# Kernel tuning notes

Hardware: AMD Instinct MI355X
Metric: run time of the kernel (lower is better)

Reference implementation:

```python
import jax, jax.numpy as jnp
import numpy as np

GROUP_SIZE = 64
M, K, N, RANK = 4096, 4096, 4096, 32


def setup_inputs() -> dict:
    key = jax.random.key(0)
    ks = jax.random.split(key, 7)
    x = jax.random.normal(ks[0], (M, K), dtype=jnp.float32)
    # int4 weight residual in [-8, 7]
    q_w = jax.random.randint(ks[1], (K, N), -8, 8, dtype=jnp.int32)
    # positive per-group weight scales, shape (K // group_size, N)
    wscales = jax.random.uniform(ks[2], (K // GROUP_SIZE, N), dtype=jnp.float32) * 0.01 + 1e-4
    lora_down = jax.random.normal(ks[3], (K, RANK), dtype=jnp.float32) * 0.02
    lora_up = jax.random.normal(ks[4], (RANK, N), dtype=jnp.float32) * 0.02
    # smoothing factors, strictly positive
    smooth = jax.random.uniform(ks[5], (K,), dtype=jnp.float32) + 0.5
    bias = jax.random.normal(ks[6], (N,), dtype=jnp.float32)
    return {"x": x, "q_w": q_w, "wscales": wscales, "lora_down": lora_down,
            "lora_up": lora_up, "smooth": smooth, "bias": bias}


def reference(x, q_w, wscales, lora_down, lora_up, smooth, bias):
    G = GROUP_SIZE
    m, k = x.shape
    n = q_w.shape[1]
    ng = k // G  # groups along K

    # smooth activation: move outliers into weights
    x_smooth = x / smooth[None, :]

    # per-group symmetric int4 quantize + dequantize of activations
    xg = x_smooth.reshape(m, ng, G)
    ascales = jnp.maximum(jnp.max(jnp.abs(xg), axis=-1) / 7.0, 1e-8)  # (m, ng)
    qx = jnp.clip(jnp.round(xg / ascales[..., None]), -8.0, 7.0)
    x_dq = (qx * ascales[..., None]).reshape(m, k)

    # dequantize int4 weight residual: grouped along K
    W_dq = (q_w.astype(jnp.float32).reshape(ng, G, n) * wscales[:, None, :]).reshape(k, n)

    # simulated int4 GEMM + fp LoRA residual + bias
    y_main = x_dq @ W_dq
    y_lora = (x @ lora_down) @ lora_up
    return y_main + y_lora + bias[None, :]
```

## Files before the change

### kernel.cpp

```cpp
#include <hip/hip_runtime.h>
#include <hip/hip_bf16.h>
#include <stdint.h>

#define GSIZE 64
#define MDIM 4096
#define KDIM 4096
#define NDIM 4096
#define RANK 32
#define KE   4160
#define NG   64
#define NSPLIT 8

#define N_LORAT (32 * NSPLIT)
#define B_WPREP0 N_LORAT
#define N_WPREP (65 * 64)
#define B_QUANT0 (B_WPREP0 + N_WPREP)
#define NBLOCKS  (B_QUANT0 + MDIM)

typedef __bf16 bf16x4 __attribute__((ext_vector_type(4)));
typedef __bf16 bf16x8 __attribute__((ext_vector_type(8)));
typedef float  f32x4  __attribute__((ext_vector_type(4)));

#define GPTR(p) ((__attribute__((address_space(1))) void*)(uintptr_t)(p))
#define LPTR(p) ((__attribute__((address_space(3))) void*)(p))

__global__ __launch_bounds__(256) void k_prep(const float* __restrict__ x,
                                              const int*   __restrict__ qw,
                                              const float* __restrict__ wsc,
                                              const float* __restrict__ ld,
                                              const float* __restrict__ lu,
                                              const float* __restrict__ smooth,
                                              __bf16* __restrict__ A,
                                              __bf16* __restrict__ Wt,
                                              float* __restrict__ tws) {
    __shared__ __attribute__((aligned(16))) char smem[10240];
    int b   = blockIdx.x;
    int tid = threadIdx.x;

    if (b < N_LORAT) {
        __bf16* AsL = (__bf16*)smem;
        __bf16* BsL = (__bf16*)(smem + 8192);
        int m0    = (b & 31) * 128;
        int sp    = b >> 5;
        int kbase = sp * 512;
        int lane = tid & 63;
        int wave = tid >> 6;
        int quad = lane >> 4;
        int mrow = lane & 15;

        f32x4 z = {0.f, 0.f, 0.f, 0.f};
        f32x4 acc[2][2];
        acc[0][0] = z; acc[0][1] = z; acc[1][0] = z; acc[1][1] = z;

        for (int step = 0; step < 16; ++step) {
            int kk = kbase + step * 32;
            #pragma unroll
            for (int it = 0; it < 2; ++it) {
                int slot = it * 256 + tid;
                int r = slot >> 2;
                int g = (slot & 3) ^ (r & 3);
                const float* src = x + (size_t)(m0 + r) * KDIM + kk + g * 8;
                float4 a0 = *(const float4*)src;
                float4 a1 = *(const float4*)(src + 4);
                bf16x8 v = {(__bf16)a0.x, (__bf16)a0.y, (__bf16)a0.z, (__bf16)a0.w,
                            (__bf16)a1.x, (__bf16)a1.y, (__bf16)a1.z, (__bf16)a1.w};
                *(bf16x8*)(AsL + slot * 8) = v;
            }
            #pragma unroll
            for (int i2 = 0; i2 < 4; ++i2) {
                int j = i2 * 256 + tid;
                int r = j >> 5, n = j & 31;
                BsL[n * 32 + r] = (__bf16)ld[(size_t)(kk + r) * RANK + n];
            }
            __syncthreads();
            bf16x8 av[2], bv[2];
            #pragma unroll
            for (int i = 0; i < 2; ++i) {
                int row  = wave * 32 + i * 16 + mrow;
                int slot = row * 4 + (quad ^ (row & 3));
                av[i] = *(const bf16x8*)(AsL + slot * 8);
            }
            #pragma unroll
            for (int j = 0; j < 2; ++j)
                bv[j] = *(const bf16x8*)(BsL + (j * 16 + mrow) * 32 + quad * 8);
            #pragma unroll
            for (int i = 0; i < 2; ++i)
                #pragma unroll
                for (int j = 0; j < 2; ++j)
                    acc[i][j] = __builtin_amdgcn_mfma_f32_16x16x32_bf16(av[i], bv[j], acc[i][j], 0, 0, 0);
            __syncthreads();
        }
        float* tout = tws + (size_t)sp * MDIM * RANK;
        #pragma unroll
        for (int i = 0; i < 2; ++i)
            #pragma unroll
            for (int j = 0; j < 2; ++j)
                #pragma unroll
                for (int r = 0; r < 4; ++r) {
                    int rowg = m0 + wave * 32 + i * 16 + quad * 4 + r;
                    int col  = j * 16 + mrow;
                    tout[(size_t)rowg * RANK + col] = acc[i][j][r];
                }
        return;
    }

    if (b < B_QUANT0) {
        __bf16 (*tile)[68] = (__bf16(*)[68])smem;
        int idx = b - B_WPREP0;
        int n0 = (idx & 63) * 64;
        int kt = idx >> 6;
        int k0 = kt * 64;
        int tr = tid >> 4;
        int tc = (tid & 15) * 4;
        if (kt < NG) {
            float4 ws = *(const float4*)(wsc + (size_t)kt * NDIM + n0 + tc);
            #pragma unroll
            for (int r = tr; r < 64; r += 16) {
                int4 q = *(const int4*)(qw + (size_t)(k0 + r) * NDIM + n0 + tc);
                tile[r][tc + 0] = (__bf16)((float)q.x * ws.x);
                tile[r][tc + 1] = (__bf16)((float)q.y * ws.y);
                tile[r][tc + 2] = (__bf16)((float)q.z * ws.z);
                tile[r][tc + 3] = (__bf16)((float)q.w * ws.w);
            }
        } else {
            #pragma unroll
            for (int r = tr; r < 64; r += 16) {
                if (r < RANK) {
                    float4 lv = *(const float4*)(lu + (size_t)r * NDIM + n0 + tc);
                    tile[r][tc + 0] = (__bf16)lv.x;
                    tile[r][tc + 1] = (__bf16)lv.y;
                    tile[r][tc + 2] = (__bf16)lv.z;
                    tile[r][tc + 3] = (__bf16)lv.w;
                } else {
                    tile[r][tc + 0] = (__bf16)0.f;
                    tile[r][tc + 1] = (__bf16)0.f;
                    tile[r][tc + 2] = (__bf16)0.f;
                    tile[r][tc + 3] = (__bf16)0.f;
                }
            }
        }
        __syncthreads();
        int nn = tid >> 3;
        int ks = (tid & 7) * 8;
        #pragma unroll
        for (int p = 0; p < 2; ++p) {
            int n = nn + p * 32;
            bf16x8 v;
            #pragma unroll
            for (int e = 0; e < 8; ++e) v[e] = tile[ks + e][n];
            *(bf16x8*)(Wt + (size_t)(n0 + n) * KE + k0 + ks) = v;
        }
        return;
    }

    {
        int row = b - B_QUANT0;
        const float4* xr4 = (const float4*)(x + (size_t)row * KDIM);
        const float4* sm4 = (const float4*)smooth;
        __bf16* ar = A + (size_t)row * KE;
        #pragma unroll
        for (int p = 0; p < 4; ++p) {
            int i4 = p * 256 + tid;
            float4 xv = xr4[i4];
            float4 sv = sm4[i4];
            float4 xs = {xv.x * __builtin_amdgcn_rcpf(sv.x),
                         xv.y * __builtin_amdgcn_rcpf(sv.y),
                         xv.z * __builtin_amdgcn_rcpf(sv.z),
                         xv.w * __builtin_amdgcn_rcpf(sv.w)};
            float a = fmaxf(fmaxf(fabsf(xs.x), fabsf(xs.y)),
                            fmaxf(fabsf(xs.z), fabsf(xs.w)));
            #pragma unroll
            for (int off = 1; off < 16; off <<= 1)
                a = fmaxf(a, __shfl_xor(a, off, 64));
            float ascale = fmaxf(a * (1.0f / 7.0f), 1e-8f);
            float rin = __builtin_amdgcn_rcpf(ascale);
            float q0 = fminf(fmaxf(rintf(xs.x * rin), -8.f), 7.f);
            float q1 = fminf(fmaxf(rintf(xs.y * rin), -8.f), 7.f);
            float q2 = fminf(fmaxf(rintf(xs.z * rin), -8.f), 7.f);
            float q3 = fminf(fmaxf(rintf(xs.w * rin), -8.f), 7.f);
            bf16x4 av = {(__bf16)(q0 * ascale), (__bf16)(q1 * ascale),
                         (__bf16)(q2 * ascale), (__bf16)(q3 * ascale)};
            *(bf16x4*)(ar + i4 * 4) = av;
        }
    }
}

__global__ __launch_bounds__(256) void k_fin(const float* __restrict__ tws,
                                             __bf16* __restrict__ A) {
    int idx = blockIdx.x * 256 + threadIdx.x;
    int m = idx >> 4, cq = idx & 15;
    int c = cq * 4;
    bf16x4 v = {(__bf16)0.f, (__bf16)0.f, (__bf16)0.f, (__bf16)0.f};
    if (c < RANK) {
        f32x4 s = {0.f, 0.f, 0.f, 0.f};
        #pragma unroll
        for (int sp = 0; sp < NSPLIT; ++sp) {
            f32x4 p = *(const f32x4*)(tws + ((size_t)sp * MDIM + m) * RANK + c);
            s.x += p.x; s.y += p.y; s.z += p.z; s.w += p.w;
        }
        v[0] = (__bf16)s.x; v[1] = (__bf16)s.y; v[2] = (__bf16)s.z; v[3] = (__bf16)s.w;
    }
    *(bf16x4*)(A + (size_t)m * KE + KDIM + c) = v;
}

__global__ __launch_bounds__(256) void k_gemm(const __bf16* __restrict__ A,
                                              const __bf16* __restrict__ Wt,
                                              const float*  __restrict__ bias,
                                              float* __restrict__ out) {
    __shared__ __attribute__((aligned(16))) __bf16 As[128 * 64];
    __shared__ __attribute__((aligned(16))) __bf16 Bs[128 * 64];
    int tid  = threadIdx.x;
    int lane = tid & 63;
    int wave = tid >> 6;
    int quad = lane >> 4;
    int mrow = lane & 15;
    int wm = wave >> 1, wn = wave & 1;
    int m0 = blockIdx.y * 128, n0 = blockIdx.x * 128;

    f32x4 z = {0.f, 0.f, 0.f, 0.f};
    f32x4 acc[4][4];
    #pragma unroll
    for (int i = 0; i < 4; ++i)
        #pragma unroll
        for (int j = 0; j < 4; ++j) acc[i][j] = z;

    const __bf16* Ab = A  + (size_t)m0 * KE;
    const __bf16* Bb = Wt + (size_t)n0 * KE;

    for (int kt = 0; kt < KE / 64; ++kt) {
        int k0 = kt * 64;
        #pragma unroll
        for (int it = 0; it < 4; ++it) {
            int c = it * 256 + tid;
            int r = c >> 3;
            int g = (c & 7) ^ (r & 7);
            int ldsoff = (it * 256 + wave * 64) * 16;
            __builtin_amdgcn_global_load_lds(GPTR(Ab + (size_t)r * KE + k0 + g * 8),
                                             LPTR((char*)As + ldsoff), 16, 0, 0);
            __builtin_amdgcn_global_load_lds(GPTR(Bb + (size_t)r * KE + k0 + g * 8),
                                             LPTR((char*)Bs + ldsoff), 16, 0, 0);
        }
        __syncthreads();
        #pragma unroll
        for (int s = 0; s < 2; ++s) {
            bf16x8 av[4], bv[4];
            #pragma unroll
            for (int i = 0; i < 4; ++i) {
                int row  = wm * 64 + i * 16 + mrow;
                int slot = row * 8 + ((s * 4 + quad) ^ (row & 7));
                av[i] = *(const bf16x8*)(As + slot * 8);
            }
            #pragma unroll
            for (int j = 0; j < 4; ++j) {
                int row  = wn * 64 + j * 16 + mrow;
                int slot = row * 8 + ((s * 4 + quad) ^ (row & 7));
                bv[j] = *(const bf16x8*)(Bs + slot * 8);
            }
            #pragma unroll
            for (int i = 0; i < 4; ++i)
                #pragma unroll
                for (int j = 0; j < 4; ++j)
                    acc[i][j] = __builtin_amdgcn_mfma_f32_16x16x32_bf16(av[i], bv[j], acc[i][j], 0, 0, 0);
        }
        __syncthreads();
    }

    #pragma unroll
    for (int j = 0; j < 4; ++j) {
        int col = n0 + wn * 64 + j * 16 + mrow;
        float bvs = bias[col];
        #pragma unroll
        for (int i = 0; i < 4; ++i) {
            int rbase = m0 + wm * 64 + i * 16 + quad * 4;
            #pragma unroll
            for (int r = 0; r < 4; ++r)
                __builtin_nontemporal_store(acc[i][j][r] + bvs,
                                            &out[(size_t)(rbase + r) * NDIM + col]);
        }
    }
}

extern "C" void kernel_launch(void* const* d_in, const int* in_sizes, int n_in,
                              void* d_out, int out_size, void* d_ws, size_t ws_size,
                              hipStream_t stream) {
    const float* x    = (const float*)d_in[0];
    const int*   qw   = (const int*)  d_in[1];
    const float* wsc  = (const float*)d_in[2];
    const float* ld   = (const float*)d_in[3];
    const float* lu   = (const float*)d_in[4];
    const float* sm   = (const float*)d_in[5];
    const float* bias = (const float*)d_in[6];
    float* out = (float*)d_out;

    char* ws = (char*)d_ws;
    __bf16* A   = (__bf16*)ws;
    __bf16* Wt  = (__bf16*)(ws + (size_t)MDIM * KE * 2);
    float*  tws = (float*) (ws + (size_t)MDIM * KE * 4);

    k_prep<<<NBLOCKS, 256, 0, stream>>>(x, qw, wsc, ld, lu, sm, A, Wt, tws);
    k_fin<<<(MDIM * 16) / 256, 256, 0, stream>>>(tws, A);
    k_gemm<<<dim3(NDIM / 128, MDIM / 128), 256, 0, stream>>>(A, Wt, bias, out);
}
```

Before: 342.0 us.

## Restructure GEMM into 256x256 tiles with double-buffered, phase-interleaved LDS prefetch

The bf16 GEMM moves from 128x128 tiles with 4 waves and a load-sync-compute loop to 256x256 tiles with 8 waves. Each k-step is split into four quadrant phases, and the global-to-LDS loads for the next two k-steps are issued between phases. This double-buffers LDS and overlaps memory with MFMA work using explicit vmcnt waits, barriers and setprio. It cuts global traffic per FLOP, at the cost of 128KB of LDS, heavier register use and fragile hand-tuned synchronisation.

```diff
diff --git a/kernel.cpp b/kernel.cpp
--- a/kernel.cpp
+++ b/kernel.cpp
@@ -203,81 +203,131 @@
     *(bf16x4*)(A + (size_t)m * KE + KDIM + c) = v;
 }
 
-__global__ __launch_bounds__(256) void k_gemm(const __bf16* __restrict__ A,
-                                              const __bf16* __restrict__ Wt,
-                                              const float*  __restrict__ bias,
-                                              float* __restrict__ out) {
-    __shared__ __attribute__((aligned(16))) __bf16 As[128 * 64];
-    __shared__ __attribute__((aligned(16))) __bf16 Bs[128 * 64];
+#define NT (KE / 64)
+#define HS 8192
+#define BS 16384
+
+#define STAGE(ldsbase, gb, kt, half) do {                                     \
+    int _k0 = (kt) * 64;                                                      \
+    _Pragma("unroll")                                                         \
+    for (int _it = 0; _it < 2; ++_it) {                                       \
+        int _c = _it * 512 + tid;                                             \
+        int _r = _c >> 3;                                                     \
+        int _g = (_c & 7) ^ (_r & 7);                                         \
+        __builtin_amdgcn_global_load_lds(                                     \
+            GPTR((gb) + (size_t)((half) * 128 + _r) * KE + _k0 + _g * 8),     \
+            LPTR((char*)(ldsbase) + (_it * 512 + wave * 64) * 16),            \
+            16, 0, 0);                                                        \
+    } } while (0)
+
+#define PHASE(qm, qn, STAGECODE, TAILWAIT) do {                               \
+    bf16x8 _av[2][4], _bv[2][2];                                              \
+    _Pragma("unroll")                                                         \
+    for (int _i = 0; _i < 4; ++_i) {                                          \
+        int _row = (qm) * 128 + wm * 64 + _i * 16 + mrow;                     \
+        _av[0][_i] = *(const bf16x8*)((const char*)Acur + _row * 128 + ga0 * 16); \
+        _av[1][_i] = *(const bf16x8*)((const char*)Acur + _row * 128 + ga1 * 16); \
+    }                                                                         \
+    _Pragma("unroll")                                                         \
+    for (int _j = 0; _j < 2; ++_j) {                                          \
+        int _row = (qn) * 128 + wn * 32 + _j * 16 + mrow;                     \
+        _bv[0][_j] = *(const bf16x8*)((const char*)Bcur + _row * 128 + ga0 * 16); \
+        _bv[1][_j] = *(const bf16x8*)((const char*)Bcur + _row * 128 + ga1 * 16); \
+    }                                                                         \
+    STAGECODE;                                                                \
+    __builtin_amdgcn_s_barrier();                                             \
+    asm volatile("s_waitcnt lgkmcnt(0)" ::: "memory");                        \
+    __builtin_amdgcn_sched_barrier(0);                                        \
+    __builtin_amdgcn_s_setprio(1);                                            \
+    _Pragma("unroll")                                                         \
+    for (int _i = 0; _i < 4; ++_i)                                            \
+        _Pragma("unroll")                                                     \
+        for (int _j = 0; _j < 2; ++_j) {                                      \
+            acc[qm][qn][_i][_j] = __builtin_amdgcn_mfma_f32_16x16x32_bf16(    \
+                _av[0][_i], _bv[0][_j], acc[qm][qn][_i][_j], 0, 0, 0);        \
+            acc[qm][qn][_i][_j] = __builtin_amdgcn_mfma_f32_16x16x32_bf16(    \
+                _av[1][_i], _bv[1][_j], acc[qm][qn][_i][_j], 0, 0, 0);        \
+        }                                                                     \
+    __builtin_amdgcn_s_setprio(0);                                            \
+    TAILWAIT;                                                                 \
+    __builtin_amdgcn_s_barrier(); } while (0)
+
+__global__ __launch_bounds__(512, 2) void k_gemm(const __bf16* __restrict__ A,
+                                                 const __bf16* __restrict__ Wt,
+                                                 const float*  __restrict__ bias,
+                                                 float* __restrict__ out) {
+    __shared__ __attribute__((aligned(16))) __bf16 As[2 * BS];
+    __shared__ __attribute__((aligned(16))) __bf16 Bs[2 * BS];
     int tid  = threadIdx.x;
     int lane = tid & 63;
     int wave = tid >> 6;
     int quad = lane >> 4;
     int mrow = lane & 15;
-    int wm = wave >> 1, wn = wave & 1;
-    int m0 = blockIdx.y * 128, n0 = blockIdx.x * 128;
-
-    f32x4 z = {0.f, 0.f, 0.f, 0.f};
-    f32x4 acc[4][4];
-    #pragma unroll
-    for (int i = 0; i < 4; ++i)
-        #pragma unroll
-        for (int j = 0; j < 4; ++j) acc[i][j] = z;
+    int wm = wave >> 2;
+    int wn = wave & 3;
+    int m0 = blockIdx.y * 256, n0 = blockIdx.x * 256;
 
     const __bf16* Ab = A  + (size_t)m0 * KE;
     const __bf16* Bb = Wt + (size_t)n0 * KE;
 
-    for (int kt = 0; kt < KE / 64; ++kt) {
-        int k0 = kt * 64;
-        #pragma unroll
-        for (int it = 0; it < 4; ++it) {
-            int c = it * 256 + tid;
-            int r = c >> 3;
-            int g = (c & 7) ^ (r & 7);
-            int ldsoff = (it * 256 + wave * 64) * 16;
-            __builtin_amdgcn_global_load_lds(GPTR(Ab + (size_t)r * KE + k0 + g * 8),
-                                             LPTR((char*)As + ldsoff), 16, 0, 0);
-            __builtin_amdgcn_global_load_lds(GPTR(Bb + (size_t)r * KE + k0 + g * 8),
-                                             LPTR((char*)Bs + ldsoff), 16, 0, 0);
-        }
-        __syncthreads();
-        #pragma unroll
-        for (int s = 0; s < 2; ++s) {
-            bf16x8 av[4], bv[4];
-            #pragma unroll
-            for (int i = 0; i < 4; ++i) {
-                int row  = wm * 64 + i * 16 + mrow;
-                int slot = row * 8 + ((s * 4 + quad) ^ (row & 7));
-                av[i] = *(const bf16x8*)(As + slot * 8);
-            }
-            #pragma unroll
-            for (int j = 0; j < 4; ++j) {
-                int row  = wn * 64 + j * 16 + mrow;
-                int slot = row * 8 + ((s * 4 + quad) ^ (row & 7));
-                bv[j] = *(const bf16x8*)(Bs + slot * 8);
-            }
+    int ga0 = quad ^ (mrow & 7);
+    int ga1 = (quad + 4) ^ (mrow & 7);
+
+    f32x4 z = {0.f, 0.f, 0.f, 0.f};
+    f32x4 acc[2][2][4][2];
+    #pragma unroll
+    for (int a = 0; a < 2; ++a)
+        #pragma unroll
+        for (int b = 0; b < 2; ++b)
             #pragma unroll
             for (int i = 0; i < 4; ++i)
                 #pragma unroll
-                for (int j = 0; j < 4; ++j)
-                    acc[i][j] = __builtin_amdgcn_mfma_f32_16x16x32_bf16(av[i], bv[j], acc[i][j], 0, 0, 0);
-        }
-        __syncthreads();
+                for (int j = 0; j < 2; ++j) acc[a][b][i][j] = z;
+
+    STAGE(As,           Ab, 0, 0);
+    STAGE(Bs + HS,      Bb, 0, 1);
+    STAGE(Bs,           Bb, 0, 0);
+    STAGE(As + HS,      Ab, 0, 1);
+    STAGE(As + BS,      Ab, 1, 0);
+    STAGE(Bs + BS + HS, Bb, 1, 1);
+    asm volatile("s_waitcnt vmcnt(4)" ::: "memory");
+    __builtin_amdgcn_s_barrier();
+
+    for (int t = 0; t < NT; ++t) {
+        int cur = t & 1;
+        const __bf16* Acur = As + cur * BS;
+        const __bf16* Bcur = Bs + cur * BS;
+        __bf16* Anx = As + (cur ^ 1) * BS;
+        __bf16* Bnx = Bs + (cur ^ 1) * BS;
+        __bf16* Acu = As + cur * BS;
+        __bf16* Bcu = Bs + cur * BS;
+        bool s1 = (t + 1 < NT), s2 = (t + 2 < NT);
+
+        PHASE(0, 0, { if (s1) STAGE(Bnx,      Bb, t + 1, 0); }, {});
+        PHASE(0, 1, { if (s1) STAGE(Anx + HS, Ab, t + 1, 1); }, {});
+        PHASE(1, 1, { if (s2) STAGE(Acu,      Ab, t + 2, 0); }, {});
+        PHASE(1, 0, { if (s2) STAGE(Bcu + HS, Bb, t + 2, 1); },
+              { if (s2) { asm volatile("s_waitcnt vmcnt(4)" ::: "memory"); }
+                else    { asm volatile("s_waitcnt vmcnt(0)" ::: "memory"); } });
     }
 
     #pragma unroll
-    for (int j = 0; j < 4; ++j) {
-        int col = n0 + wn * 64 + j * 16 + mrow;
-        float bvs = bias[col];
-        #pragma unroll
-        for (int i = 0; i < 4; ++i) {
-            int rbase = m0 + wm * 64 + i * 16 + quad * 4;
-            #pragma unroll
-            for (int r = 0; r < 4; ++r)
-                __builtin_nontemporal_store(acc[i][j][r] + bvs,
-                                            &out[(size_t)(rbase + r) * NDIM + col]);
-        }
-    }
+    for (int qn = 0; qn < 2; ++qn)
+        #pragma unroll
+        for (int j = 0; j < 2; ++j) {
+            int col = n0 + qn * 128 + wn * 32 + j * 16 + mrow;
+            float bvs = bias[col];
+            #pragma unroll
+            for (int qm = 0; qm < 2; ++qm)
+                #pragma unroll
+                for (int i = 0; i < 4; ++i) {
+                    int rbase = m0 + qm * 128 + wm * 64 + i * 16 + quad * 4;
+                    #pragma unroll
+                    for (int r = 0; r < 4; ++r)
+                        __builtin_nontemporal_store(acc[qm][qn][i][j][r] + bvs,
+                                                    &out[(size_t)(rbase + r) * NDIM + col]);
+                }
+        }
 }
 
 extern "C" void kernel_launch(void* const* d_in, const int* in_sizes, int n_in,
@@ -299,5 +349,5 @@
 
     k_prep<<<NBLOCKS, 256, 0, stream>>>(x, qw, wsc, ld, lu, sm, A, Wt, tws);
     k_fin<<<(MDIM * 16) / 256, 256, 0, stream>>>(tws, A);
-    k_gemm<<<dim3(NDIM / 128, MDIM / 128), 256, 0, stream>>>(A, Wt, bias, out);
+    k_gemm<<<dim3(NDIM / 256, MDIM / 256), 512, 0, stream>>>(A, Wt, bias, out);
 }
```

Result: slower. 356.8 us (+4.3%).
